# Kernel optimization log

Measured on AMD Instinct MI355X. Metric: run time of the kernel, lower is better.

## Reference

```python
import jax, jax.numpy as jnp
import numpy as np

D_IN = 768      # inp_dim
NH = 8          # head_num
HD = 96         # head_dim
HID = NH * HD   # 768
UP = 2 * D_IN   # p_factor[0]=2.0 -> 1536
FUSED = 2 * NH + 3 * HID  # 2320
KER = 4
CS = 64         # chunk_size
CAP = 15.0      # gate_soft_cap
EPS = 1e-6


def _ln(x, w, b):
    m = jnp.mean(x, -1, keepdims=True)
    v = jnp.mean((x - m) ** 2, -1, keepdims=True)
    return (x - m) / jnp.sqrt(v + EPS) * w + b


def setup_inputs() -> dict:
    key = jax.random.key(0)
    ks = jax.random.split(key, 10)
    B, S = 2, 4096
    def lin(k, fin, fout):
        return (jax.random.normal(k, (fin, fout), jnp.float32) / np.sqrt(fin)).astype(jnp.float32)
    return {
        "x": jax.random.normal(ks[0], (B, S, D_IN), jnp.float32),
        "ln_in_w": jnp.ones((D_IN,), jnp.float32), "ln_in_b": jnp.zeros((D_IN,), jnp.float32),
        "ln_hid_w": jnp.ones((HID,), jnp.float32), "ln_hid_b": jnp.zeros((HID,), jnp.float32),
        "up_l_w": lin(ks[1], D_IN, UP), "up_l_b": jnp.zeros((UP,), jnp.float32),
        "up_r_w": lin(ks[2], D_IN, HID), "up_r_b": jnp.zeros((HID,), jnp.float32),
        "down_w": lin(ks[3], HID, D_IN), "down_b": jnp.zeros((D_IN,), jnp.float32),
        "conv_w": (jax.random.normal(ks[4], (KER,), jnp.float32) * 0.5).astype(jnp.float32),
        "conv_b": jnp.zeros((), jnp.float32),
        "skip_w": lin(ks[5], UP, HID), "skip_b": jnp.zeros((HID,), jnp.float32),
        "fused_w": lin(ks[6], UP, FUSED), "fused_b": jnp.zeros((FUSED,), jnp.float32),
        "wo_w": lin(ks[7], UP, HID), "wo_b": jnp.zeros((HID,), jnp.float32),
    }


def reference(x, ln_in_w, ln_in_b, ln_hid_w, ln_hid_b, up_l_w, up_l_b, up_r_w, up_r_b,
              down_w, down_b, conv_w, conv_b, skip_w, skip_b, fused_w, fused_b, wo_w, wo_b):
    B, S, _ = x.shape
    soft_cap = lambda t: CAP * jnp.tanh(t / CAP)

    x_n = _ln(x, ln_in_w, ln_in_b)
    x_t = x_n @ up_l_w + up_l_b          # [B,S,UP]
    r_t = x_n @ up_r_w + up_r_b          # [B,S,HID]

    # causal conv: single shared (1,1,KER) kernel, depthwise across UP channels
    xp = jnp.pad(x_t, ((0, 0), (KER - 1, 0), (0, 0)))
    x_c = conv_b + sum(conv_w[j] * xp[:, j:j + S, :] for j in range(KER))
    x_c = jax.nn.silu(x_c)

    x_skip = x_c @ skip_w + skip_b
    proj = x_c @ fused_w + fused_b
    i_pre = soft_cap(proj[..., :NH])
    f_pre = soft_cap(proj[..., NH:2 * NH])
    q, k, v = jnp.split(proj[..., 2 * NH:], 3, axis=-1)
    o = jax.nn.sigmoid(x_t @ wo_w + wo_b)

    resh = lambda t: t.reshape(B, S, NH, HD).transpose(0, 2, 1, 3)  # [B,NH,S,HD]
    q = resh(q)
    k = resh(k) / np.sqrt(HD)
    v = resh(v)

    i_g = i_pre.transpose(0, 2, 1)  # [B,NH,S]
    f_g = f_pre.transpose(0, 2, 1)
    mx = jnp.maximum(f_g, i_g)
    i_g = jnp.exp(i_g - mx)
    f_g = jnp.exp(f_g - mx)

    NC = S // CS
    qc = q.reshape(B, NH, NC, CS, HD)
    kc = k.reshape(B, NH, NC, CS, HD)
    vc = v.reshape(B, NH, NC, CS, HD)
    ic = i_g.reshape(B, NH, NC, CS)
    fc = f_g.reshape(B, NH, NC, CS)

    lf = jnp.cumsum(jnp.log(fc + 1e-8), -1)          # [B,NH,NC,CS]
    f_cumul = jnp.exp(lf - lf[..., -1:])
    wC = f_cumul * ic
    # inter-chunk states; final_forget = exp(lf[-1]-lf[-1]) == 1 exactly -> exclusive cumsum
    C_contrib = jnp.einsum('bncl,bncld,bncle->bncde', wC, vc, kc)  # v-outer-k
    n_contrib = jnp.einsum('bncl,bncld->bncd', wC, kc)
    C_init = jnp.concatenate([jnp.zeros_like(C_contrib[:, :, :1]),
                              jnp.cumsum(C_contrib, axis=2)[:, :, :-1]], axis=2)
    n_init = jnp.concatenate([jnp.zeros_like(n_contrib[:, :, :1]),
                              jnp.cumsum(n_contrib, axis=2)[:, :, :-1]], axis=2)

    # intra-chunk, strictly-causal (j < i)
    mask = jnp.tril(jnp.ones((CS, CS), bool), -1)
    dl = lf[..., :, None] - lf[..., None, :]
    w = jnp.where(mask, ic[..., None, :] * jnp.exp(jnp.where(mask, dl, 0.0)), 0.0)
    scores = jnp.einsum('bncid,bncjd->bncij', qc, kc)
    attn = jax.nn.softmax(jnp.where(mask, scores, -1e30), axis=-1)
    attn = jnp.where(mask, attn, 0.0)  # pos 0 row -> all zeros

    h_intra = jnp.einsum('bncij,bncjd->bncid', attn * w, vc)
    n_intra = jnp.einsum('bncij,bncjd->bncid', w, kc)
    h_init = jnp.einsum('bncde,bncie->bncid', C_init, qc)

    total_n = n_init[..., None, :] + n_intra
    denom = jnp.maximum(jnp.sum(total_n * qc, -1, keepdims=True), 1.0)
    h = (h_init + h_intra) / denom                    # [B,NH,NC,CS,HD]

    h = h.reshape(B, NH, S, HD).transpose(0, 2, 1, 3).reshape(B, S, HID)
    h = o * h
    out = _ln(h, ln_hid_w, ln_hid_b) + x_skip
    out = out * jax.nn.silu(r_t)
    out = out @ down_w + down_b
    return out + x
```

## Files before the change

kernel.cpp:

```cpp
#include <hip/hip_runtime.h>
#include <hip/hip_bf16.h>
#include <math.h>

#define D_IN  768
#define NHD   8
#define HDIM  96
#define HID   768
#define UPD   1536
#define FUSED 2320
#define KER   4
#define CS    64
#define NCH   64
#define SB    4096
#define BB    2
#define NROW  (BB*SB)
#define NCHUNK (BB*NHD*NCH)

using u16   = unsigned short;
using frag8 = __attribute__((ext_vector_type(8))) short;
using f32x4 = __attribute__((ext_vector_type(4))) float;

#define O_WUPL   0
#define O_WUPR   1769472
#define O_WSKIP  2359296
#define O_WFUS   3538944
#define O_WWO    9142272
#define O_WDOWN  10321920
#define O_RT     10911744
#define O_XSKIP  17203200
#define O_LF     23494656
#define O_IC     23560192
#define O_WC     23625728
#define O_NC     23691264
#define O_XN     23789568
#define O_XT     33226752
#define O_XTS    45809664
#define O_PROJ   23789568
#define O_CC     23789568
#define O_H      33226752
#define O_OUT1   39518208

__device__ __forceinline__ void gld_lds16u(const u16* g, u16* l) {
    __builtin_amdgcn_global_load_lds(
        (const __attribute__((address_space(1))) void*)g,
        (__attribute__((address_space(3))) void*)l, 16, 0, 0);
}

__device__ __forceinline__ void split3u(float f, unsigned &H, unsigned &M, unsigned &L) {
    unsigned u = __float_as_uint(f);
    unsigned hr = (u + 0x7fffu + ((u >> 16) & 1u)) & 0xffff0000u;
    H = hr;
    float rm = f - __uint_as_float(hr);
    unsigned mr = __float_as_uint(rm) & 0xffff0000u;
    M = mr;
    float rl = rm - __uint_as_float(mr);
    L = __float_as_uint(rl) & 0xffff0000u;
}

__global__ __launch_bounds__(256) void tpose_split(
    const float* __restrict__ w, u16* __restrict__ tH, u16* __restrict__ tM,
    u16* __restrict__ tL, int K, int N)
{
    __shared__ float tile[64][65];
    int k0 = blockIdx.x * 64, n0 = blockIdx.y * 64;
    int t = threadIdx.x;
    int c = t & 63, r4 = t >> 6;
    #pragma unroll
    for (int it = 0; it < 16; ++it) {
        int r = r4 + it * 4;
        int n = n0 + c;
        tile[r][c] = (n < N) ? w[(size_t)(k0 + r) * N + n] : 0.f;
    }
    __syncthreads();
    #pragma unroll
    for (int it = 0; it < 16; ++it) {
        int nn = r4 + it * 4;
        float v = tile[c][nn];
        unsigned H, M, L;
        split3u(v, H, M, L);
        size_t idx = (size_t)(n0 + nn) * K + k0 + c;
        tH[idx] = (u16)(H >> 16);
        tM[idx] = (u16)(M >> 16);
        if (tL) tL[idx] = (u16)(L >> 16);
    }
}

__global__ __launch_bounds__(256) void ln_in_split(
    const float* __restrict__ x, const float* __restrict__ w,
    const float* __restrict__ b, u16* __restrict__ oH,
    u16* __restrict__ oM, u16* __restrict__ oL)
{
    int row = blockIdx.x;
    size_t base = (size_t)row * D_IN;
    int c0 = threadIdx.x, c1 = threadIdx.x + 256, c2 = threadIdx.x + 512;
    float v0 = x[base + c0], v1 = x[base + c1], v2 = x[base + c2];
    float s = v0 + v1 + v2;
    float ss = v0*v0 + v1*v1 + v2*v2;
    for (int off = 32; off; off >>= 1) { s += __shfl_xor(s, off); ss += __shfl_xor(ss, off); }
    __shared__ float red[8];
    int wid = threadIdx.x >> 6;
    if ((threadIdx.x & 63) == 0) { red[wid] = s; red[4 + wid] = ss; }
    __syncthreads();
    s = red[0] + red[1] + red[2] + red[3];
    ss = red[4] + red[5] + red[6] + red[7];
    float mean = s * (1.f / D_IN);
    float var = ss * (1.f / D_IN) - mean * mean;
    float inv = rsqrtf(var + 1e-6f);
    float r0 = (v0 - mean) * inv * w[c0] + b[c0];
    float r1 = (v1 - mean) * inv * w[c1] + b[c1];
    float r2 = (v2 - mean) * inv * w[c2] + b[c2];
    unsigned H, M, L;
    split3u(r0, H, M, L); oH[base+c0]=(u16)(H>>16); oM[base+c0]=(u16)(M>>16); oL[base+c0]=(u16)(L>>16);
    split3u(r1, H, M, L); oH[base+c1]=(u16)(H>>16); oM[base+c1]=(u16)(M>>16); oL[base+c1]=(u16)(L>>16);
    split3u(r2, H, M, L); oH[base+c2]=(u16)(H>>16); oM[base+c2]=(u16)(M>>16); oL[base+c2]=(u16)(L>>16);
}

template<int NT, int NTH>
__global__ __launch_bounds__(NTH) void gemm_sp(
    const u16* __restrict__ aH, const u16* __restrict__ aM, const u16* __restrict__ aL,
    const u16* __restrict__ bH, const u16* __restrict__ bM, const u16* __restrict__ bL,
    const float* __restrict__ bias, const float* __restrict__ resid,
    float* __restrict__ C, u16* __restrict__ cH, u16* __restrict__ cM,
    int N, int K, int act)
{
    constexpr int BM = (NT == 6) ? 256 : 128;
    constexpr int NW = NTH / 64;
    __shared__ u16 AHM[2][BM * 64];
    __shared__ u16 BHM[2][128 * 64];
    __shared__ u16 ALp[(NT == 6) ? 2 : 1][(NT == 6) ? 128 * 64 : 8];
    __shared__ u16 BLp[(NT == 6) ? 2 : 1][(NT == 6) ? 64 * 64 : 8];

    int t = threadIdx.x;
    int wave = t >> 6, lane = t & 63;
    int lin = blockIdx.y * gridDim.x + blockIdx.x;
    int cpx = (gridDim.x * gridDim.y) >> 3;
    int sw  = (lin & 7) * cpx + (lin >> 3);
    int bx = sw % gridDim.x, by = sw / gridDim.x;
    int m0 = by * BM, n0 = bx * 128;

    int wm, wn;
    if constexpr (NT == 6) { wm = (wave >> 1) * 64; wn = (wave & 1) * 64; }
    else                   { wm = (wave >> 1) * 64; wn = (wave & 1) * 64; }
    f32x4 acc[4][4] = {};

    int l7 = lane & 7, l8 = lane >> 3;
    int lc = l7 ^ l8;
    int lane15 = lane & 15, rsel = lane >> 4;
    int pH = (rsel ^ l7) * 8;
    int pM = ((4 | rsel) ^ l7) * 8;
    int aLrow = (lane15 >> 1) * 64 + (((((lane & 1) << 2) | rsel) ^ (lane15 >> 1)) * 8);
    int wslot = wave;

    auto stage = [&](int buf, int k0) {
        if constexpr (NT == 6) {
            #pragma unroll
            for (int j = 0; j < 4; ++j) {
                int g = j * 8 + wslot;
                int r = g * 8 + l8;
                const u16* src = (lc >= 4 ? aM : aH) + (size_t)(m0 + r) * K + k0 + (lc & 3) * 8;
                gld_lds16u(src, &AHM[buf][g * 512 + lane * 8]);
            }
            #pragma unroll
            for (int j = 0; j < 2; ++j) {
                int g = j * 8 + wslot;
                int r = g * 8 + l8;
                const u16* src = (lc >= 4 ? bM : bH) + (size_t)(n0 + r) * K + k0 + (lc & 3) * 8;
                gld_lds16u(src, &BHM[buf][g * 512 + lane * 8]);
            }
            #pragma unroll
            for (int j = 0; j < 2; ++j) {
                int g = j * 8 + wslot;
                int R = g * 8 + l8;
                int rr = 2 * R + (lc >> 2);
                const u16* src = aL + (size_t)(m0 + rr) * K + k0 + (lc & 3) * 8;
                gld_lds16u(src, &ALp[buf][g * 512 + lane * 8]);
            }
            {
                int g = wslot;
                int R = g * 8 + l8;
                int rr = 2 * R + (lc >> 2);
                const u16* src = bL + (size_t)(n0 + rr) * K + k0 + (lc & 3) * 8;
                gld_lds16u(src, &BLp[buf][g * 512 + lane * 8]);
            }
        } else {
            #pragma unroll
            for (int j = 0; j < 4; ++j) {
                int g = j * 4 + wslot;
                int r = g * 8 + l8;
                const u16* src = (lc >= 4 ? aM : aH) + (size_t)(m0 + r) * K + k0 + (lc & 3) * 8;
                gld_lds16u(src, &AHM[buf][g * 512 + lane * 8]);
            }
            #pragma unroll
            for (int j = 0; j < 4; ++j) {
                int g = j * 4 + wslot;
                int r = g * 8 + l8;
                const u16* src = (lc >= 4 ? bM : bH) + (size_t)(n0 + r) * K + k0 + (lc & 3) * 8;
                gld_lds16u(src, &BHM[buf][g * 512 + lane * 8]);
            }
        }
    };

    auto compute = [&](int buf) {
        frag8 ah[4], am[4], al[(NT == 6) ? 4 : 1];
        #pragma unroll
        for (int mi = 0; mi < 4; ++mi) {
            int rr = wm + mi * 16 + lane15;
            const u16* bp = &AHM[buf][rr * 64];
            ah[mi] = *(const frag8*)&bp[pH];
            am[mi] = *(const frag8*)&bp[pM];
            if constexpr (NT == 6)
                al[mi] = *(const frag8*)&ALp[buf][(wm >> 1) * 64 + mi * 512 + aLrow];
        }
        #pragma unroll
        for (int ni = 0; ni < 4; ++ni) {
            int rb = wn + ni * 16 + lane15;
            const u16* bp = &BHM[buf][rb * 64];
            frag8 bh = *(const frag8*)&bp[pH];
            frag8 bm = *(const frag8*)&bp[pM];
            if constexpr (NT == 6) {
                frag8 bl = *(const frag8*)&BLp[buf][(wn >> 1) * 64 + ni * 512 + aLrow];
                #pragma unroll
                for (int mi = 0; mi < 4; ++mi) {
                    acc[mi][ni] = __builtin_amdgcn_mfma_f32_16x16x32_bf16(ah[mi], bm, acc[mi][ni], 0, 0, 0);
                    acc[mi][ni] = __builtin_amdgcn_mfma_f32_16x16x32_bf16(am[mi], bh, acc[mi][ni], 0, 0, 0);
                    acc[mi][ni] = __builtin_amdgcn_mfma_f32_16x16x32_bf16(ah[mi], bl, acc[mi][ni], 0, 0, 0);
                    acc[mi][ni] = __builtin_amdgcn_mfma_f32_16x16x32_bf16(al[mi], bh, acc[mi][ni], 0, 0, 0);
                    acc[mi][ni] = __builtin_amdgcn_mfma_f32_16x16x32_bf16(am[mi], bm, acc[mi][ni], 0, 0, 0);
                    acc[mi][ni] = __builtin_amdgcn_mfma_f32_16x16x32_bf16(ah[mi], bh, acc[mi][ni], 0, 0, 0);
                }
            } else {
                #pragma unroll
                for (int mi = 0; mi < 4; ++mi) {
                    acc[mi][ni] = __builtin_amdgcn_mfma_f32_16x16x32_bf16(ah[mi], bm, acc[mi][ni], 0, 0, 0);
                    acc[mi][ni] = __builtin_amdgcn_mfma_f32_16x16x32_bf16(am[mi], bh, acc[mi][ni], 0, 0, 0);
                    acc[mi][ni] = __builtin_amdgcn_mfma_f32_16x16x32_bf16(ah[mi], bh, acc[mi][ni], 0, 0, 0);
                }
            }
        }
    };

    int ns = K >> 5;
    stage(0, 0);
    asm volatile("" ::: "memory");
    int cur = 0;
    for (int s = 0; s < ns - 1; ++s) {
        stage(cur ^ 1, (s + 1) * 32);
        if constexpr (NT == 6) asm volatile("s_waitcnt vmcnt(9)" ::: "memory");
        else                   asm volatile("s_waitcnt vmcnt(8)" ::: "memory");
        __builtin_amdgcn_sched_barrier(0);
        __builtin_amdgcn_s_barrier();
        compute(cur);
        __builtin_amdgcn_s_barrier();
        cur ^= 1;
    }
    asm volatile("s_waitcnt vmcnt(0)" ::: "memory");
    __builtin_amdgcn_sched_barrier(0);
    __builtin_amdgcn_s_barrier();
    compute(cur);

    const bool dosplit = (cH != nullptr);
    #pragma unroll
    for (int ni = 0; ni < 4; ++ni) {
        int ncol = n0 + wn + ni * 16 + (lane & 15);
        if (ncol >= N) continue;
        float bs = bias[ncol];
        #pragma unroll
        for (int mi = 0; mi < 4; ++mi) {
            #pragma unroll
            for (int r = 0; r < 4; ++r) {
                int mrow = m0 + wm + mi * 16 + (lane >> 4) * 4 + r;
                float val = acc[mi][ni][r] + bs;
                if (act == 1) val = 1.f / (1.f + expf(-val));
                if (resid) val += resid[(size_t)mrow * N + ncol];
                C[(size_t)mrow * N + ncol] = val;
                if (dosplit) {
                    unsigned H, M, L;
                    split3u(val, H, M, L);
                    cH[(size_t)mrow * N + ncol] = (u16)(H >> 16);
                    cM[(size_t)mrow * N + ncol] = (u16)(M >> 16);
                }
            }
        }
    }
}

__global__ void conv_split(const float* __restrict__ xt, const float* __restrict__ cw,
                           const float* __restrict__ cb, u16* __restrict__ xcH,
                           u16* __restrict__ xcM, u16* __restrict__ xcL)
{
    size_t idx = (size_t)blockIdx.x * blockDim.x + threadIdx.x;
    if (idx >= (size_t)NROW * UPD) return;
    int ch = idx % UPD;
    int s = (int)((idx / UPD) % SB);
    int b = (int)(idx / ((size_t)UPD * SB));
    float acc = cb[0];
    #pragma unroll
    for (int j = 0; j < KER; ++j) {
        int sj = s - (KER - 1) + j;
        if (sj >= 0) acc += cw[j] * xt[((size_t)b * SB + sj) * UPD + ch];
    }
    float v = acc / (1.f + expf(-acc));
    unsigned H, M, L;
    split3u(v, H, M, L);
    xcH[idx] = (u16)(H >> 16);
    xcM[idx] = (u16)(M >> 16);
    xcL[idx] = (u16)(L >> 16);
}

__global__ __launch_bounds__(64) void gates_kernel(
    const float* __restrict__ proj, float* __restrict__ lf,
    float* __restrict__ ic, float* __restrict__ wC)
{
    int cid = blockIdx.x;
    int l = threadIdx.x;
    int b = cid >> 9;
    int nh = (cid >> 6) & 7;
    int c = cid & 63;
    int s = c * CS + l;
    size_t row = ((size_t)b * SB + s) * FUSED;
    float ip = proj[row + nh];
    float fp = proj[row + NHD + nh];
    ip = 15.f * tanhf(ip * (1.f / 15.f));
    fp = 15.f * tanhf(fp * (1.f / 15.f));
    float mx = fmaxf(ip, fp);
    float ig = expf(ip - mx);
    float fg = expf(fp - mx);
    float v = logf(fg + 1e-8f);
    for (int off = 1; off < 64; off <<= 1) {
        float u = __shfl_up(v, off);
        if (l >= off) v += u;
    }
    float last = __shfl(v, 63);
    lf[cid * CS + l] = v;
    ic[cid * CS + l] = ig;
    wC[cid * CS + l] = expf(v - last) * ig;
}

__global__ void repack_kernel(const float* __restrict__ proj, float* __restrict__ q,
                              float* __restrict__ k, float* __restrict__ v)
{
    size_t idx = (size_t)blockIdx.x * blockDim.x + threadIdx.x;
    if (idx >= (size_t)BB * NHD * NCH * CS * HDIM) return;
    int d = idx % HDIM; size_t r1 = idx / HDIM;
    int l = r1 % CS; r1 /= CS;
    int c = r1 % NCH; r1 /= NCH;
    int nh = r1 % NHD; int b = (int)(r1 / NHD);
    size_t row = ((size_t)b * SB + c * CS + l) * FUSED + 2 * NHD + nh * HDIM + d;
    q[idx] = proj[row];
    k[idx] = proj[row + HID] * 0.10206207261596577f;
    v[idx] = proj[row + 2 * HID];
}

__global__ __launch_bounds__(256) void chunk_outer_kernel(
    const float* __restrict__ k, const float* __restrict__ v,
    const float* __restrict__ wC, float* __restrict__ Cc, float* __restrict__ nc)
{
    __shared__ float kL[CS * HDIM], vL[CS * HDIM], wL[CS];
    int cid = blockIdx.x, t = threadIdx.x;
    const float* kg = k + (size_t)cid * CS * HDIM;
    const float* vg = v + (size_t)cid * CS * HDIM;
    for (int idx = t; idx < CS * HDIM; idx += 256) { kL[idx] = kg[idx]; vL[idx] = vg[idx]; }
    if (t < CS) wL[t] = wC[cid * CS + t];
    __syncthreads();
    int eb = t >> 3;
    int db = t & 7;
    float4 acc[3][3];
    #pragma unroll
    for (int e2 = 0; e2 < 3; ++e2)
        #pragma unroll
        for (int x = 0; x < 3; ++x) acc[e2][x] = make_float4(0.f, 0.f, 0.f, 0.f);
    for (int l = 0; l < CS; ++l) {
        float w = wL[l];
        float wk[3];
        #pragma unroll
        for (int e2 = 0; e2 < 3; ++e2) wk[e2] = w * kL[l * HDIM + 3 * eb + e2];
        const float* vr = &vL[l * HDIM + 12 * db];
        float4 vv[3];
        #pragma unroll
        for (int x = 0; x < 3; ++x) vv[x] = *(const float4*)(vr + 4 * x);
        #pragma unroll
        for (int e2 = 0; e2 < 3; ++e2)
            #pragma unroll
            for (int x = 0; x < 3; ++x) {
                acc[e2][x].x += wk[e2] * vv[x].x;
                acc[e2][x].y += wk[e2] * vv[x].y;
                acc[e2][x].z += wk[e2] * vv[x].z;
                acc[e2][x].w += wk[e2] * vv[x].w;
            }
    }
    float* Cb = Cc + (size_t)cid * HDIM * HDIM;
    #pragma unroll
    for (int e2 = 0; e2 < 3; ++e2)
        #pragma unroll
        for (int x = 0; x < 3; ++x)
            *(float4*)&Cb[(size_t)(3 * eb + e2) * HDIM + 12 * db + 4 * x] = acc[e2][x];
    if (t < HDIM) {
        float acc2 = 0.f;
        for (int l = 0; l < CS; ++l) acc2 += wL[l] * kL[l * HDIM + t];
        nc[(size_t)cid * HDIM + t] = acc2;
    }
}

__global__ void scan_kernel(float* __restrict__ Cc, float* __restrict__ nc)
{
    int gid = blockIdx.x * blockDim.x + threadIdx.x;
    const int NCE = BB * NHD * HDIM * HDIM;
    if (gid < NCE) {
        int bh = gid / (HDIM * HDIM);
        int ent = gid % (HDIM * HDIM);
        float run = 0.f;
        float* base = Cc + (size_t)bh * NCH * HDIM * HDIM + ent;
        for (int c = 0; c < NCH; ++c) {
            float tv = base[(size_t)c * HDIM * HDIM];
            base[(size_t)c * HDIM * HDIM] = run;
            run += tv;
        }
    } else {
        int g2 = gid - NCE;
        if (g2 < BB * NHD * HDIM) {
            int bh = g2 / HDIM, ent = g2 % HDIM;
            float run = 0.f;
            float* base = nc + (size_t)bh * NCH * HDIM + ent;
            for (int c = 0; c < NCH; ++c) {
                float tv = base[c * HDIM];
                base[c * HDIM] = run;
                run += tv;
            }
        }
    }
}

__global__ __launch_bounds__(256) void attn_kernel(
    const float* __restrict__ q, const float* __restrict__ k, const float* __restrict__ v,
    const float* __restrict__ lf, const float* __restrict__ ic,
    const float* __restrict__ CiT, const float* __restrict__ ni,
    float* __restrict__ hout)
{
    __shared__ float qL[64 * 100];
    __shared__ float kL[64 * 100];
    __shared__ float lfL[64], icL[64], niL[96];
    int cid = blockIdx.x, t = threadIdx.x;
    int b = cid >> 9, nh = (cid >> 6) & 7, c = cid & 63;
    const float* qg = q + (size_t)cid * (CS * HDIM);
    const float* kg = k + (size_t)cid * (CS * HDIM);
    const float* vg = v + (size_t)cid * (CS * HDIM);
    const float4* qg4 = (const float4*)qg;
    const float4* kg4 = (const float4*)kg;
    #pragma unroll
    for (int it = 0; it < 6; ++it) {
        int idx = t + it * 256;
        int row = idx / 24, col = (idx % 24) * 4;
        *(float4*)&qL[row * 100 + col] = qg4[idx];
        *(float4*)&kL[row * 100 + col] = kg4[idx];
    }
    if (t < 64) { lfL[t] = lf[cid * CS + t]; icL[t] = ic[cid * CS + t]; }
    else if (t < 160) { niL[t - 64] = ni[(size_t)cid * HDIM + (t - 64)]; }
    __syncthreads();

    int i = t >> 2, g = t & 3;
    const float* qrow = qL + i * 100;
    float sc[16];
    #pragma unroll
    for (int jj = 0; jj < 16; ++jj) sc[jj] = 0.f;
    for (int d4 = 0; d4 < 24; ++d4) {
        float4 qv = *(const float4*)(qrow + 4 * d4);
        #pragma unroll
        for (int jj = 0; jj < 16; ++jj) {
            float4 kv = *(const float4*)(kL + (g + 4 * jj) * 100 + 4 * d4);
            sc[jj] += qv.x * kv.x + qv.y * kv.y + qv.z * kv.z + qv.w * kv.w;
        }
    }
    float lfi = lfL[i];
    float wv[16];
    #pragma unroll
    for (int jj = 0; jj < 16; ++jj) {
        int j = g + 4 * jj;
        wv[jj] = (j < i) ? icL[j] * expf(lfi - lfL[j]) : 0.f;
    }
    float den = 0.f;
    #pragma unroll
    for (int jj = 0; jj < 16; ++jj) den += wv[jj] * sc[jj];
    #pragma unroll
    for (int dd = 0; dd < 24; ++dd) {
        int d = 24 * g + dd;
        den += niL[d] * qrow[d];
    }
    float m = -1e30f;
    #pragma unroll
    for (int jj = 0; jj < 16; ++jj) { int j = g + 4 * jj; if (j < i) m = fmaxf(m, sc[jj]); }
    m = fmaxf(m, __shfl_xor(m, 1)); m = fmaxf(m, __shfl_xor(m, 2));
    float p = 0.f;
    #pragma unroll
    for (int jj = 0; jj < 16; ++jj) {
        int j = g + 4 * jj;
        sc[jj] = (j < i) ? expf(sc[jj] - m) : 0.f;
        p += sc[jj];
    }
    p += __shfl_xor(p, 1); p += __shfl_xor(p, 2);
    float pinv = (p > 0.f) ? 1.f / p : 0.f;
    __syncthreads();
    float* awL = kL;
    #pragma unroll
    for (int jj = 0; jj < 16; ++jj) {
        int j = g + 4 * jj;
        awL[i * 68 + j] = sc[jj] * pinv * wv[jj];
    }
    __syncthreads();
    float4 h4[6];
    #pragma unroll
    for (int x = 0; x < 6; ++x) h4[x] = make_float4(0.f, 0.f, 0.f, 0.f);
    const float* vbase = vg + 24 * g;
    for (int j = 0; j < 64; ++j) {
        float a = awL[i * 68 + j];
        const float4* vr = (const float4*)(vbase + j * HDIM);
        #pragma unroll
        for (int x = 0; x < 6; ++x) {
            float4 vv = vr[x];
            h4[x].x += a * vv.x; h4[x].y += a * vv.y; h4[x].z += a * vv.z; h4[x].w += a * vv.w;
        }
    }
    const float* Cb = CiT + (size_t)cid * (HDIM * HDIM) + 24 * g;
    for (int e = 0; e < 96; ++e) {
        float qe = qrow[e];
        const float4* cr = (const float4*)(Cb + e * HDIM);
        #pragma unroll
        for (int x = 0; x < 6; ++x) {
            float4 cv = cr[x];
            h4[x].x += qe * cv.x; h4[x].y += qe * cv.y; h4[x].z += qe * cv.z; h4[x].w += qe * cv.w;
        }
    }
    den += __shfl_xor(den, 1); den += __shfl_xor(den, 2);
    float dinv = 1.f / fmaxf(den, 1.f);
    int s = c * CS + i;
    float4* hr4 = (float4*)(hout + (((size_t)b * SB + s) * NHD + nh) * HDIM + 24 * g);
    #pragma unroll
    for (int x = 0; x < 6; ++x) {
        float4 hv;
        hv.x = h4[x].x * dinv; hv.y = h4[x].y * dinv;
        hv.z = h4[x].z * dinv; hv.w = h4[x].w * dinv;
        hr4[x] = hv;
    }
}

__global__ __launch_bounds__(256) void ln_hid_split(
    const float* __restrict__ h, const float* __restrict__ o,
    const float* __restrict__ xskip, const float* __restrict__ rt,
    const float* __restrict__ w, const float* __restrict__ bb,
    u16* __restrict__ oH, u16* __restrict__ oM)
{
    int row = blockIdx.x;
    size_t base = (size_t)row * HID;
    int c0 = threadIdx.x, c1 = threadIdx.x + 256, c2 = threadIdx.x + 512;
    float v0 = o[base + c0] * h[base + c0];
    float v1 = o[base + c1] * h[base + c1];
    float v2 = o[base + c2] * h[base + c2];
    float s = v0 + v1 + v2;
    float ss = v0*v0 + v1*v1 + v2*v2;
    for (int off = 32; off; off >>= 1) { s += __shfl_xor(s, off); ss += __shfl_xor(ss, off); }
    __shared__ float red[8];
    int wid = threadIdx.x >> 6;
    if ((threadIdx.x & 63) == 0) { red[wid] = s; red[4 + wid] = ss; }
    __syncthreads();
    s = red[0] + red[1] + red[2] + red[3];
    ss = red[4] + red[5] + red[6] + red[7];
    float mean = s * (1.f / HID);
    float var = ss * (1.f / HID) - mean * mean;
    float inv = rsqrtf(var + 1e-6f);
    float g0 = rt[base + c0], g1 = rt[base + c1], g2 = rt[base + c2];
    float r0 = ((v0 - mean) * inv * w[c0] + bb[c0] + xskip[base + c0]) * (g0 / (1.f + expf(-g0)));
    float r1 = ((v1 - mean) * inv * w[c1] + bb[c1] + xskip[base + c1]) * (g1 / (1.f + expf(-g1)));
    float r2 = ((v2 - mean) * inv * w[c2] + bb[c2] + xskip[base + c2]) * (g2 / (1.f + expf(-g2)));
    unsigned H, M, L;
    split3u(r0, H, M, L); oH[base+c0]=(u16)(H>>16); oM[base+c0]=(u16)(M>>16);
    split3u(r1, H, M, L); oH[base+c1]=(u16)(H>>16); oM[base+c1]=(u16)(M>>16);
    split3u(r2, H, M, L); oH[base+c2]=(u16)(H>>16); oM[base+c2]=(u16)(M>>16);
}

extern "C" void kernel_launch(void* const* d_in, const int* in_sizes, int n_in,
                              void* d_out, int out_size, void* d_ws, size_t ws_size,
                              hipStream_t stream)
{
    const float* x       = (const float*)d_in[0];
    const float* ln_in_w = (const float*)d_in[1];
    const float* ln_in_b = (const float*)d_in[2];
    const float* ln_hid_w= (const float*)d_in[3];
    const float* ln_hid_b= (const float*)d_in[4];
    const float* up_l_w  = (const float*)d_in[5];
    const float* up_l_b  = (const float*)d_in[6];
    const float* up_r_w  = (const float*)d_in[7];
    const float* up_r_b  = (const float*)d_in[8];
    const float* down_w  = (const float*)d_in[9];
    const float* down_b  = (const float*)d_in[10];
    const float* conv_w  = (const float*)d_in[11];
    const float* conv_b  = (const float*)d_in[12];
    const float* skip_w  = (const float*)d_in[13];
    const float* skip_b  = (const float*)d_in[14];
    const float* fused_w = (const float*)d_in[15];
    const float* fused_b = (const float*)d_in[16];
    const float* wo_w    = (const float*)d_in[17];
    const float* wo_b    = (const float*)d_in[18];
    float* out = (float*)d_out;

    float* ws = (float*)d_ws;
    u16* wuplH = (u16*)(ws + O_WUPL);  u16* wuplM = wuplH + 1179648; u16* wuplL = wuplM + 1179648;
    u16* wuprH = (u16*)(ws + O_WUPR);  u16* wuprM = wuprH + 589824;
    u16* wskpH = (u16*)(ws + O_WSKIP); u16* wskpM = wskpH + 1179648;
    u16* wfusH = (u16*)(ws + O_WFUS);  u16* wfusM = wfusH + 3735552; u16* wfusL = wfusM + 3735552;
    u16* wwoH  = (u16*)(ws + O_WWO);   u16* wwoM  = wwoH  + 1179648;
    u16* wdwnH = (u16*)(ws + O_WDOWN); u16* wdwnM = wdwnH + 589824;
    float* rt    = ws + O_RT;
    float* xskip = ws + O_XSKIP;
    float* lf    = ws + O_LF;
    float* ic    = ws + O_IC;
    float* wC    = ws + O_WC;
    float* nc    = ws + O_NC;
    u16* xnH = (u16*)(ws + O_XN);  u16* xnM = xnH + 6291456; u16* xnL = xnM + 6291456;
    float* xt = ws + O_XT;
    u16* xtH = (u16*)(ws + O_XTS); u16* xtM = xtH + 12582912;
    u16* xcH = (u16*)(ws + O_XTS); u16* xcM = xcH + 12582912; u16* xcL = xcM + 12582912;
    float* proj = ws + O_PROJ;
    float* q = ws + O_XTS;
    float* k = ws + O_XTS + 6291456;
    float* v = ws + O_XTS + 12582912;
    float* Cc = ws + O_CC;
    float* h  = ws + O_H;
    u16* out1H = (u16*)(ws + O_OUT1); u16* out1M = out1H + 6291456;
    float* o = (float*)d_out;

    tpose_split<<<dim3(12, 24), 256, 0, stream>>>(up_l_w, wuplH, wuplM, wuplL, 768, 1536);
    tpose_split<<<dim3(12, 12), 256, 0, stream>>>(up_r_w, wuprH, wuprM, nullptr, 768, 768);
    tpose_split<<<dim3(24, 12), 256, 0, stream>>>(skip_w, wskpH, wskpM, nullptr, 1536, 768);
    tpose_split<<<dim3(24, 38), 256, 0, stream>>>(fused_w, wfusH, wfusM, wfusL, 1536, 2320);
    tpose_split<<<dim3(24, 12), 256, 0, stream>>>(wo_w, wwoH, wwoM, nullptr, 1536, 768);
    tpose_split<<<dim3(12, 12), 256, 0, stream>>>(down_w, wdwnH, wdwnM, nullptr, 768, 768);
    ln_in_split<<<NROW, 256, 0, stream>>>(x, ln_in_w, ln_in_b, xnH, xnM, xnL);
    gemm_sp<6,512><<<dim3(12, 32), 512, 0, stream>>>(xnH, xnM, xnL, wuplH, wuplM, wuplL,
        up_l_b, nullptr, xt, xtH, xtM, UPD, D_IN, 0);
    gemm_sp<3,256><<<dim3(6, 64), 256, 0, stream>>>(xnH, xnM, nullptr, wuprH, wuprM, nullptr,
        up_r_b, nullptr, rt, nullptr, nullptr, HID, D_IN, 0);
    gemm_sp<3,256><<<dim3(6, 64), 256, 0, stream>>>(xtH, xtM, nullptr, wwoH, wwoM, nullptr,
        wo_b, nullptr, o, nullptr, nullptr, HID, UPD, 1);
    {
        size_t tot = (size_t)NROW * UPD;
        conv_split<<<(unsigned)((tot + 255) / 256), 256, 0, stream>>>(xt, conv_w, conv_b, xcH, xcM, xcL);
    }
    gemm_sp<3,256><<<dim3(6, 64), 256, 0, stream>>>(xcH, xcM, nullptr, wskpH, wskpM, nullptr,
        skip_b, nullptr, xskip, nullptr, nullptr, HID, UPD, 0);
    gemm_sp<6,512><<<dim3(19, 32), 512, 0, stream>>>(xcH, xcM, xcL, wfusH, wfusM, wfusL,
        fused_b, nullptr, proj, nullptr, nullptr, FUSED, UPD, 0);
    gates_kernel<<<NCHUNK, 64, 0, stream>>>(proj, lf, ic, wC);
    {
        size_t tot = (size_t)BB * NHD * NCH * CS * HDIM;
        repack_kernel<<<(unsigned)((tot + 255) / 256), 256, 0, stream>>>(proj, q, k, v);
    }
    chunk_outer_kernel<<<NCHUNK, 256, 0, stream>>>(k, v, wC, Cc, nc);
    {
        int tot = BB * NHD * HDIM * HDIM + BB * NHD * HDIM;
        scan_kernel<<<(tot + 255) / 256, 256, 0, stream>>>(Cc, nc);
    }
    attn_kernel<<<NCHUNK, 256, 0, stream>>>(q, k, v, lf, ic, Cc, nc, h);
    ln_hid_split<<<NROW, 256, 0, stream>>>(h, o, xskip, rt, ln_hid_w, ln_hid_b, out1H, out1M);
    gemm_sp<3,256><<<dim3(6, 64), 256, 0, stream>>>(out1H, out1M, nullptr, wdwnH, wdwnM, nullptr,
        down_b, x, out, nullptr, nullptr, D_IN, HID, 0);
}
```

Before: 1.258 ms.

## Restructure GEMM main loop into barrier-separated MFMA clusters with priority boosts

The GEMM inner loop is reorganised so each K step runs four phases. Each phase loads one B fragment from LDS, synchronises, then issues its MFMA cluster at raised wave priority (s_setprio). The previous double-buffered loop waited on a partial vmcnt before each compute; the new loop waits for all global loads at the end of each step. The aim is to interleave LDS reads with MFMA work across waves in a ping-pong style schedule. In exchange it adds several barriers per step and drains global loads fully every iteration, which may reduce overlap of global prefetch.

```diff
diff --git a/kernel.cpp b/kernel.cpp
--- a/kernel.cpp
+++ b/kernel.cpp
@@ -124,7 +124,6 @@
     int N, int K, int act)
 {
     constexpr int BM = (NT == 6) ? 256 : 128;
-    constexpr int NW = NTH / 64;
     __shared__ u16 AHM[2][BM * 64];
     __shared__ u16 BHM[2][128 * 64];
     __shared__ u16 ALp[(NT == 6) ? 2 : 1][(NT == 6) ? 128 * 64 : 8];
@@ -138,9 +137,7 @@
     int bx = sw % gridDim.x, by = sw / gridDim.x;
     int m0 = by * BM, n0 = bx * 128;
 
-    int wm, wn;
-    if constexpr (NT == 6) { wm = (wave >> 1) * 64; wn = (wave & 1) * 64; }
-    else                   { wm = (wave >> 1) * 64; wn = (wave & 1) * 64; }
+    int wm = (wave >> 1) * 64, wn = (wave & 1) * 64;
     f32x4 acc[4][4] = {};
 
     int l7 = lane & 7, l8 = lane >> 3;
@@ -200,8 +197,9 @@
         }
     };
 
-    auto compute = [&](int buf) {
-        frag8 ah[4], am[4], al[(NT == 6) ? 4 : 1];
+    frag8 ah[4], am[4], al[(NT == 6) ? 4 : 1];
+
+    auto loadA = [&](int buf) {
         #pragma unroll
         for (int mi = 0; mi < 4; ++mi) {
             int rr = wm + mi * 16 + lane15;
@@ -211,52 +209,77 @@
             if constexpr (NT == 6)
                 al[mi] = *(const frag8*)&ALp[buf][(wm >> 1) * 64 + mi * 512 + aLrow];
         }
-        #pragma unroll
-        for (int ni = 0; ni < 4; ++ni) {
-            int rb = wn + ni * 16 + lane15;
-            const u16* bp = &BHM[buf][rb * 64];
-            frag8 bh = *(const frag8*)&bp[pH];
-            frag8 bm = *(const frag8*)&bp[pM];
-            if constexpr (NT == 6) {
-                frag8 bl = *(const frag8*)&BLp[buf][(wn >> 1) * 64 + ni * 512 + aLrow];
-                #pragma unroll
-                for (int mi = 0; mi < 4; ++mi) {
-                    acc[mi][ni] = __builtin_amdgcn_mfma_f32_16x16x32_bf16(ah[mi], bm, acc[mi][ni], 0, 0, 0);
-                    acc[mi][ni] = __builtin_amdgcn_mfma_f32_16x16x32_bf16(am[mi], bh, acc[mi][ni], 0, 0, 0);
-                    acc[mi][ni] = __builtin_amdgcn_mfma_f32_16x16x32_bf16(ah[mi], bl, acc[mi][ni], 0, 0, 0);
-                    acc[mi][ni] = __builtin_amdgcn_mfma_f32_16x16x32_bf16(al[mi], bh, acc[mi][ni], 0, 0, 0);
-                    acc[mi][ni] = __builtin_amdgcn_mfma_f32_16x16x32_bf16(am[mi], bm, acc[mi][ni], 0, 0, 0);
-                    acc[mi][ni] = __builtin_amdgcn_mfma_f32_16x16x32_bf16(ah[mi], bh, acc[mi][ni], 0, 0, 0);
-                }
-            } else {
-                #pragma unroll
-                for (int mi = 0; mi < 4; ++mi) {
-                    acc[mi][ni] = __builtin_amdgcn_mfma_f32_16x16x32_bf16(ah[mi], bm, acc[mi][ni], 0, 0, 0);
-                    acc[mi][ni] = __builtin_amdgcn_mfma_f32_16x16x32_bf16(am[mi], bh, acc[mi][ni], 0, 0, 0);
-                    acc[mi][ni] = __builtin_amdgcn_mfma_f32_16x16x32_bf16(ah[mi], bh, acc[mi][ni], 0, 0, 0);
-                }
+    };
+    auto loadB = [&](int buf, int ni, frag8& bh, frag8& bm, frag8& bl) {
+        int rb = wn + ni * 16 + lane15;
+        const u16* bp = &BHM[buf][rb * 64];
+        bh = *(const frag8*)&bp[pH];
+        bm = *(const frag8*)&bp[pM];
+        if constexpr (NT == 6)
+            bl = *(const frag8*)&BLp[buf][(wn >> 1) * 64 + ni * 512 + aLrow];
+    };
+    auto cluster = [&](int ni, frag8 bh, frag8 bm, frag8 bl) {
+        if constexpr (NT == 6) {
+            #pragma unroll
+            for (int mi = 0; mi < 4; ++mi) {
+                acc[mi][ni] = __builtin_amdgcn_mfma_f32_16x16x32_bf16(ah[mi], bm, acc[mi][ni], 0, 0, 0);
+                acc[mi][ni] = __builtin_amdgcn_mfma_f32_16x16x32_bf16(am[mi], bh, acc[mi][ni], 0, 0, 0);
+                acc[mi][ni] = __builtin_amdgcn_mfma_f32_16x16x32_bf16(ah[mi], bl, acc[mi][ni], 0, 0, 0);
+                acc[mi][ni] = __builtin_amdgcn_mfma_f32_16x16x32_bf16(al[mi], bh, acc[mi][ni], 0, 0, 0);
+                acc[mi][ni] = __builtin_amdgcn_mfma_f32_16x16x32_bf16(am[mi], bm, acc[mi][ni], 0, 0, 0);
+                acc[mi][ni] = __builtin_amdgcn_mfma_f32_16x16x32_bf16(ah[mi], bh, acc[mi][ni], 0, 0, 0);
+            }
+        } else {
+            #pragma unroll
+            for (int mi = 0; mi < 4; ++mi) {
+                acc[mi][ni] = __builtin_amdgcn_mfma_f32_16x16x32_bf16(ah[mi], bm, acc[mi][ni], 0, 0, 0);
+                acc[mi][ni] = __builtin_amdgcn_mfma_f32_16x16x32_bf16(am[mi], bh, acc[mi][ni], 0, 0, 0);
+                acc[mi][ni] = __builtin_amdgcn_mfma_f32_16x16x32_bf16(ah[mi], bh, acc[mi][ni], 0, 0, 0);
             }
         }
     };
 
     int ns = K >> 5;
     stage(0, 0);
-    asm volatile("" ::: "memory");
-    int cur = 0;
-    for (int s = 0; s < ns - 1; ++s) {
-        stage(cur ^ 1, (s + 1) * 32);
-        if constexpr (NT == 6) asm volatile("s_waitcnt vmcnt(9)" ::: "memory");
-        else                   asm volatile("s_waitcnt vmcnt(8)" ::: "memory");
-        __builtin_amdgcn_sched_barrier(0);
-        __builtin_amdgcn_s_barrier();
-        compute(cur);
-        __builtin_amdgcn_s_barrier();
-        cur ^= 1;
-    }
     asm volatile("s_waitcnt vmcnt(0)" ::: "memory");
     __builtin_amdgcn_sched_barrier(0);
     __builtin_amdgcn_s_barrier();
-    compute(cur);
+    int cur = 0;
+    for (int s = 0; s < ns; ++s) {
+        frag8 bh, bm, bl = {};
+        if (s + 1 < ns) stage(cur ^ 1, (s + 1) * 32);
+        loadA(cur);
+        loadB(cur, 0, bh, bm, bl);
+        __builtin_amdgcn_s_barrier();
+        asm volatile("s_waitcnt lgkmcnt(0)" ::: "memory");
+        __builtin_amdgcn_sched_barrier(0);
+        __builtin_amdgcn_s_setprio(1);
+        cluster(0, bh, bm, bl);
+        __builtin_amdgcn_s_setprio(0);
+        __builtin_amdgcn_s_barrier();
+        #pragma unroll
+        for (int ni = 1; ni < 3; ++ni) {
+            loadB(cur, ni, bh, bm, bl);
+            __builtin_amdgcn_s_barrier();
+            asm volatile("s_waitcnt lgkmcnt(0)" ::: "memory");
+            __builtin_amdgcn_sched_barrier(0);
+            __builtin_amdgcn_s_setprio(1);
+            cluster(ni, bh, bm, bl);
+            __builtin_amdgcn_s_setprio(0);
+            __builtin_amdgcn_s_barrier();
+        }
+        loadB(cur, 3, bh, bm, bl);
+        __builtin_amdgcn_s_barrier();
+        asm volatile("s_waitcnt lgkmcnt(0)" ::: "memory");
+        __builtin_amdgcn_sched_barrier(0);
+        __builtin_amdgcn_s_setprio(1);
+        cluster(3, bh, bm, bl);
+        __builtin_amdgcn_s_setprio(0);
+        asm volatile("s_waitcnt vmcnt(0)" ::: "memory");
+        __builtin_amdgcn_sched_barrier(0);
+        __builtin_amdgcn_s_barrier();
+        cur ^= 1;
+    }
 
     const bool dosplit = (cH != nullptr);
     #pragma unroll
```

New measurement: 1.399 ms. +11.2%, slower.
